# Kernel tuning notes

Measured on AMD Instinct MI355X. Metric: run time of the kernel, lower is better.

## Reference

```python
import jax, jax.numpy as jnp
import numpy as np

N = 100000   # nodes
E = 1600000  # edges (avg degree 16)
D = 128      # input_dim = embedding_dim = output_dim
NEG_SLOPE = 0.01  # nn.LeakyReLU default


def setup_inputs() -> dict:
    key = jax.random.key(0)
    k0, k1, k2, k3, k4, k5 = jax.random.split(key, 6)
    x = jax.random.normal(k0, (N, D), jnp.float32)
    edge_index = jax.random.randint(k1, (2, E), 0, N, dtype=jnp.int32)
    batch = jnp.zeros((N,), jnp.int32)
    # GCNConv params (glorot-ish scale)
    W1 = jax.random.normal(k2, (D, D), jnp.float32) * 0.05
    b1 = jax.random.normal(k3, (D,), jnp.float32) * 0.05
    W2 = jax.random.normal(k4, (D, D), jnp.float32) * 0.05
    b2 = jax.random.normal(k5, (D,), jnp.float32) * 0.05
    return {"x": x, "W1": W1, "b1": b1, "W2": W2, "b2": b2,
            "edge_index": edge_index, "batch": batch}


def _gcn_conv(x, W, b, src, dst, deg_isqrt):
    # x' = D^{-1/2} (A + I) D^{-1/2} (x W) + b   (PyG GCNConv defaults)
    h = x @ W                                   # [N, D]
    coef = deg_isqrt[src] * deg_isqrt[dst]      # [E]
    msg = h[src] * coef[:, None]                # [E, D] gather + scale
    out = jax.ops.segment_sum(msg, dst, num_segments=N)  # scatter-add
    out = out + h * (deg_isqrt * deg_isqrt)[:, None]      # self-loop term
    return out + b


def reference(x, W1, b1, W2, b2, edge_index, batch):
    src, dst = edge_index[0], edge_index[1]
    # degree on A + I (self loops), same for both layers
    deg = jax.ops.segment_sum(jnp.ones((E,), x.dtype), dst, num_segments=N) + 1.0
    deg_isqrt = jax.lax.rsqrt(deg)
    h = _gcn_conv(x, W1, b1, src, dst, deg_isqrt)
    h = jax.nn.leaky_relu(h, NEG_SLOPE)
    h = _gcn_conv(h, W2, b2, src, dst, deg_isqrt)
    return jax.nn.leaky_relu(h, NEG_SLOPE)
```

## Files before the change

### kernel.cpp

```cpp
#include <hip/hip_runtime.h>
#include <hip/hip_bf16.h>
#include <stdint.h>

#define NN 100000
#define NE 1600000
#define NR (NE + NN)
#define DD 128
#define NEG 0.01f
#define NB 196
#define EPB 4096
#define NBLK1 391

typedef __attribute__((ext_vector_type(8))) short short8;
typedef __attribute__((ext_vector_type(4))) float floatx4;
typedef __attribute__((ext_vector_type(4))) uint32_t uint32x4;

__device__ __forceinline__ uint16_t f2bf(float f){
  uint32_t i = __float_as_uint(f);
  return (uint16_t)((i + 0x7FFFu + ((i >> 16) & 1u)) >> 16);
}
__device__ __forceinline__ float lrelu(float x){ return fmaxf(x, NEG * x); }

__global__ void k_detect(const uint32_t* __restrict__ xw, int* __restrict__ flag){
  int lane = threadIdx.x;
  uint32_t w = xw[lane];
  uint32_t e = (w >> 7) & 0xFFu;
  int plaus = (e >= 100u && e <= 134u) ? 1 : 0;
  unsigned long long b = __ballot(plaus);
  if (lane == 0) flag[0] = (__popcll(b) >= 48) ? 0 : 1;
}

__global__ __launch_bounds__(256) void k_hist(const int* __restrict__ dst,
                                              int* __restrict__ ghist){
  __shared__ int lh[NB];
  int t = threadIdx.x, b = blockIdx.x;
  if (t < NB) lh[t] = 0;
  __syncthreads();
  #pragma unroll
  for (int i = 0; i < 16; i++){
    int e = b * EPB + i * 256 + t;
    if (e < NE) atomicAdd(&lh[dst[e] >> 9], 1);
  }
  __syncthreads();
  if (t < NB) ghist[t * NBLK1 + b] = lh[t];
}

__global__ __launch_bounds__(512) void k_bscan(int* __restrict__ ghist,
                                               int* __restrict__ btotal){
  __shared__ int sm[512];
  int t = threadIdx.x, bkt = blockIdx.x;
  int v = (t < NBLK1) ? ghist[bkt * NBLK1 + t] : 0;
  sm[t] = v;
  __syncthreads();
  for (int s = 1; s < 512; s <<= 1){
    int add = (t >= s) ? sm[t - s] : 0;
    __syncthreads();
    sm[t] += add;
    __syncthreads();
  }
  if (t < NBLK1) ghist[bkt * NBLK1 + t] = sm[t] - v;
  if (t == 0) btotal[bkt] = sm[511];
}

__global__ __launch_bounds__(256) void k_bscan2(const int* __restrict__ btotal,
                                                int* __restrict__ bucketbase){
  __shared__ int sm[256];
  int t = threadIdx.x;
  int v = (t < NB) ? btotal[t] : 0;
  sm[t] = v;
  __syncthreads();
  for (int s = 1; s < 256; s <<= 1){
    int add = (t >= s) ? sm[t - s] : 0;
    __syncthreads();
    sm[t] += add;
    __syncthreads();
  }
  if (t < NB) bucketbase[t] = sm[t] - v;
  if (t == 0) bucketbase[NB] = sm[255];
}

__global__ __launch_bounds__(256) void k_scatter(const int* __restrict__ src,
                                                 const int* __restrict__ dst,
                                                 const int* __restrict__ ghist,
                                                 const int* __restrict__ bucketbase,
                                                 uint64_t* __restrict__ pairs){
  __shared__ int lcur[NB];
  int t = threadIdx.x, b = blockIdx.x;
  if (t < NB) lcur[t] = bucketbase[t] + ghist[t * NBLK1 + b];
  __syncthreads();
  #pragma unroll
  for (int i = 0; i < 16; i++){
    int e = b * EPB + i * 256 + t;
    if (e < NE){
      int s = src[e], d = dst[e];
      int pos = atomicAdd(&lcur[d >> 9], 1);
      pairs[pos] = ((uint64_t)(uint32_t)d << 32) | (uint32_t)s;
    }
  }
}

__global__ __launch_bounds__(512) void k_bsort(const uint64_t* __restrict__ pairs,
                                               const int* __restrict__ bucketbase,
                                               int2* __restrict__ pairs2,
                                               int* __restrict__ prowstart,
                                               float* __restrict__ dis){
  __shared__ int lcnt[512], lofs[512], sm[512];
  __shared__ float sdn[512];
  int t = threadIdx.x, bkt = blockIdx.x;
  int n0 = bkt << 9;
  int beg = bucketbase[bkt], end = bucketbase[bkt + 1];
  int begS = beg + n0;
  lcnt[t] = 0;
  __syncthreads();
  for (int i = beg + t; i < end; i += 512){
    int d = (int)(pairs[i] >> 32);
    atomicAdd(&lcnt[d - n0], 1);
  }
  __syncthreads();
  int n = n0 + t;
  int inb = (n < NN) ? 1 : 0;
  int v = lcnt[t] + inb;
  sm[t] = v;
  __syncthreads();
  for (int s = 1; s < 512; s <<= 1){
    int add = (t >= s) ? sm[t - s] : 0;
    __syncthreads();
    sm[t] += add;
    __syncthreads();
  }
  int excl = sm[t] - v;
  float dn = rsqrtf((float)(lcnt[t] + 1));
  lofs[t] = excl + 1;
  sdn[t] = dn;
  if (inb){
    prowstart[n] = begS + excl;
    dis[n] = dn;
    pairs2[begS + excl] = make_int2(n, __float_as_int(dn));
  }
  if (bkt == 0 && t == 0) prowstart[NN] = NR;
  __syncthreads();
  for (int i = beg + t; i < end; i += 512){
    uint64_t u = pairs[i];
    int d = (int)(u >> 32);
    int p = atomicAdd(&lofs[d - n0], 1);
    pairs2[begS + p] = make_int2((int)(uint32_t)u, __float_as_int(sdn[d - n0]));
  }
}

__global__ void k_prep2(int2* __restrict__ pairs2, const float* __restrict__ dis){
  int i = blockIdx.x * 256 + threadIdx.x;
  if (i < NR){
    int2 r = pairs2[i];
    r.y = __float_as_int(__int_as_float(r.y) * dis[r.x]);
    pairs2[i] = r;
  }
}

__global__ void k_wb(const void* __restrict__ W1, const void* __restrict__ W2,
                     const void* __restrict__ b1, const void* __restrict__ b2,
                     uint16_t* __restrict__ WT1, uint16_t* __restrict__ WT2,
                     uint16_t* __restrict__ bb, const int* __restrict__ flag){
  int idx = blockIdx.x * 256 + threadIdx.x;
  int f = flag[0];
  if (idx < 16384){
    int c = idx >> 7, k = idx & 127;
    WT1[idx] = f ? f2bf(((const float*)W1)[k * DD + c])
                 : ((const uint16_t*)W1)[k * DD + c];
  } else if (idx < 32768){
    int j = idx - 16384;
    int c = j >> 7, k = j & 127;
    WT2[j] = f ? f2bf(((const float*)W2)[k * DD + c])
               : ((const uint16_t*)W2)[k * DD + c];
  } else if (idx < 33024){
    int j = idx - 32768;
    const void* s = (j < 128) ? b1 : b2;
    int i2 = j & 127;
    bb[j] = f ? f2bf(((const float*)s)[i2]) : ((const uint16_t*)s)[i2];
  }
}

__device__ __forceinline__ short8 ldcvt(const float* __restrict__ p){
  floatx4 u = ((const floatx4*)p)[0], v = ((const floatx4*)p)[1];
  short8 r;
  r[0] = (short)f2bf(u.x); r[1] = (short)f2bf(u.y);
  r[2] = (short)f2bf(u.z); r[3] = (short)f2bf(u.w);
  r[4] = (short)f2bf(v.x); r[5] = (short)f2bf(v.y);
  r[6] = (short)f2bf(v.z); r[7] = (short)f2bf(v.w);
  return r;
}

__global__ __launch_bounds__(256) void k_gemm(const void* __restrict__ X,
                                              const uint16_t* __restrict__ WT,
                                              uint16_t* __restrict__ H,
                                              const int* __restrict__ flag,
                                              int xf32){
  __shared__ uint16_t lwt[128 * 136];
  int t = threadIdx.x;
  const uint32_t* wt32 = (const uint32_t*)WT;
  #pragma unroll
  for (int i = 0; i < 32; i++){
    int uidx = t + 256 * i;
    uint32_t w2 = wt32[uidx];
    int el = uidx * 2;
    int c = el >> 7, k = el & 127;
    *(uint32_t*)&lwt[c * 136 + k] = w2;
  }
  __syncthreads();

  int wave = t >> 6, lane = t & 63;
  int m = lane & 15, q = lane >> 4;
  int rowbase = blockIdx.x * 64 + wave * 16;
  int ar = rowbase + m;
  if (ar >= NN) ar = 0;
  short8 a0, a1, a2, a3;
  if (xf32 && flag[0]){
    const float* xr = (const float*)X + (size_t)ar * DD;
    a0 = ldcvt(xr + q * 8);        a1 = ldcvt(xr + (q + 4) * 8);
    a2 = ldcvt(xr + (q + 8) * 8);  a3 = ldcvt(xr + (q + 12) * 8);
  } else {
    const short8* xrow = (const short8*)((const uint16_t*)X + (size_t)ar * DD);
    a0 = xrow[q]; a1 = xrow[q + 4]; a2 = xrow[q + 8]; a3 = xrow[q + 12];
  }

  #pragma unroll
  for (int nt = 0; nt < 8; nt++){
    int c = nt * 16 + m;
    const uint16_t* bp = &lwt[c * 136 + q * 8];
    floatx4 acc = {0.f, 0.f, 0.f, 0.f};
    acc = __builtin_amdgcn_mfma_f32_16x16x32_bf16(a0, *(const short8*)(bp +  0), acc, 0, 0, 0);
    acc = __builtin_amdgcn_mfma_f32_16x16x32_bf16(a1, *(const short8*)(bp + 32), acc, 0, 0, 0);
    acc = __builtin_amdgcn_mfma_f32_16x16x32_bf16(a2, *(const short8*)(bp + 64), acc, 0, 0, 0);
    acc = __builtin_amdgcn_mfma_f32_16x16x32_bf16(a3, *(const short8*)(bp + 96), acc, 0, 0, 0);
    #pragma unroll
    for (int r = 0; r < 4; r++){
      int row = rowbase + q * 4 + r;
      if (row < NN) H[(size_t)row * DD + c] = f2bf(acc[r]);
    }
  }
}

#define FMA8(VA, CF)                                                     \
  acc[0] = fmaf(__uint_as_float(VA.x << 16),         CF, acc[0]);        \
  acc[1] = fmaf(__uint_as_float(VA.x & 0xffff0000u), CF, acc[1]);        \
  acc[2] = fmaf(__uint_as_float(VA.y << 16),         CF, acc[2]);        \
  acc[3] = fmaf(__uint_as_float(VA.y & 0xffff0000u), CF, acc[3]);        \
  acc[4] = fmaf(__uint_as_float(VA.z << 16),         CF, acc[4]);        \
  acc[5] = fmaf(__uint_as_float(VA.z & 0xffff0000u), CF, acc[5]);        \
  acc[6] = fmaf(__uint_as_float(VA.w << 16),         CF, acc[6]);        \
  acc[7] = fmaf(__uint_as_float(VA.w & 0xffff0000u), CF, acc[7]);

__global__ __launch_bounds__(256) void k_agg(const uint16_t* __restrict__ H,
                                             const int* __restrict__ prow,
                                             const int2* __restrict__ pairs2,
                                             const uint16_t* __restrict__ bias,
                                             void* __restrict__ OUT,
                                             const int* __restrict__ flag,
                                             int is_final){
  __shared__ int2 ebuf[4][68];
  int wave = threadIdx.x >> 6, lane = threadIdx.x & 63;
  int grp = lane >> 4, sl = lane & 15;
  if (lane < 4) ebuf[wave][64 + lane] = make_int2(0, 0);
  int n = blockIdx.x * 4 + wave;
  if (n >= NN) return;
  int beg = prow[n], end = prow[n + 1];

  float acc[8] = {0.f,0.f,0.f,0.f,0.f,0.f,0.f,0.f};
  for (int j0 = beg; j0 < end; j0 += 64){
    int cnt = min(64, end - j0);
    int2 r = (lane < cnt) ? pairs2[j0 + lane] : make_int2(0, 0);
    ebuf[wave][lane] = r;
    int chunks = (cnt + 3) >> 2;
    int2 ea = ebuf[wave][grp];
    uint32x4 va = *(const uint32x4*)(H + (size_t)ea.x * DD + sl * 8);
    for (int c = 0; c < chunks; c++){
      int2 eb = ebuf[wave][c * 4 + 4 + grp];
      uint32x4 vb = *(const uint32x4*)(H + (size_t)eb.x * DD + sl * 8);
      float cf = __int_as_float(ea.y);
      FMA8(va, cf)
      ea = eb; va = vb;
    }
  }
  #pragma unroll
  for (int j = 0; j < 8; j++){
    acc[j] += __shfl_xor(acc[j], 16, 64);
    acc[j] += __shfl_xor(acc[j], 32, 64);
  }
  uint32x4 bv = ((const uint32x4*)bias)[sl];
  float o0 = lrelu(acc[0] + __uint_as_float(bv.x << 16));
  float o1 = lrelu(acc[1] + __uint_as_float(bv.x & 0xffff0000u));
  float o2 = lrelu(acc[2] + __uint_as_float(bv.y << 16));
  float o3 = lrelu(acc[3] + __uint_as_float(bv.y & 0xffff0000u));
  float o4 = lrelu(acc[4] + __uint_as_float(bv.z << 16));
  float o5 = lrelu(acc[5] + __uint_as_float(bv.z & 0xffff0000u));
  float o6 = lrelu(acc[6] + __uint_as_float(bv.w << 16));
  float o7 = lrelu(acc[7] + __uint_as_float(bv.w & 0xffff0000u));
  if (is_final && flag[0]){
    float* orow = (float*)OUT + (size_t)n * DD + sl * 8;
    if (lane < 16){ floatx4 vv = {o0, o1, o2, o3}; ((floatx4*)orow)[0] = vv; }
    else if (lane < 32){ floatx4 vv = {o4, o5, o6, o7}; ((floatx4*)orow)[1] = vv; }
  } else if (lane < 16){
    uint32x4 pv;
    pv.x = (uint32_t)f2bf(o0) | ((uint32_t)f2bf(o1) << 16);
    pv.y = (uint32_t)f2bf(o2) | ((uint32_t)f2bf(o3) << 16);
    pv.z = (uint32_t)f2bf(o4) | ((uint32_t)f2bf(o5) << 16);
    pv.w = (uint32_t)f2bf(o6) | ((uint32_t)f2bf(o7) << 16);
    *(uint32x4*)((uint16_t*)OUT + (size_t)n * DD + sl * 8) = pv;
  }
}

extern "C" void kernel_launch(void* const* d_in, const int* in_sizes, int n_in,
                              void* d_out, int out_size, void* d_ws, size_t ws_size,
                              hipStream_t stream){
  const void* x  = d_in[0];
  const void* W1 = d_in[1];
  const void* b1 = d_in[2];
  const void* W2 = d_in[3];
  const void* b2 = d_in[4];
  const int* ei   = (const int*)d_in[5];
  const int* esrc = ei;
  const int* edst = ei + NE;

  char* ws = (char*)d_ws;
  float*    dis        = (float*)(ws + 0);
  int*      prow       = (int*)(ws + 512ull * 1024);
  int*      flag       = (int*)(ws + 960ull * 1024);
  uint16_t* WT1        = (uint16_t*)(ws + 964ull * 1024);
  uint16_t* WT2        = (uint16_t*)(ws + 996ull * 1024);
  uint16_t* bb         = (uint16_t*)(ws + 1028ull * 1024);
  int*      ghist      = (int*)(ws + 1032ull * 1024);
  int*      btotal     = (int*)(ws + 1344ull * 1024);
  int*      bucketbase = (int*)(ws + 1348ull * 1024);
  int2*     pairs2     = (int2*)(ws + 2048ull * 1024);
  uint64_t* pairs      = (uint64_t*)(ws + 16384ull * 1024);
  uint16_t* hA         = (uint16_t*)(ws + 16384ull * 1024);
  uint16_t* hB         = (uint16_t*)d_out;

  k_detect<<<1, 64, 0, stream>>>((const uint32_t*)x, flag);
  k_hist  <<<NBLK1, 256, 0, stream>>>(edst, ghist);
  k_bscan <<<NB, 512, 0, stream>>>(ghist, btotal);
  k_bscan2<<<1, 256, 0, stream>>>(btotal, bucketbase);
  k_scatter<<<NBLK1, 256, 0, stream>>>(esrc, edst, ghist, bucketbase, pairs);
  k_bsort <<<NB, 512, 0, stream>>>(pairs, bucketbase, pairs2, prow, dis);
  k_prep2 <<<(NR + 255) / 256, 256, 0, stream>>>(pairs2, dis);
  k_wb    <<<129, 256, 0, stream>>>(W1, W2, b1, b2, WT1, WT2, bb, flag);

  k_gemm<<<(NN + 63) / 64, 256, 0, stream>>>(x, WT1, hA, flag, 1);
  k_agg <<<NN / 4, 256, 0, stream>>>(hA, prow, pairs2, bb, hB, flag, 0);
  k_gemm<<<(NN + 63) / 64, 256, 0, stream>>>(hB, WT2, hA, flag, 0);
  k_agg <<<NN / 4, 256, 0, stream>>>(hA, prow, pairs2, bb + 128, d_out, flag, 1);
}
```

Before: 321.4 us.

## Assign one 16-lane group per node in aggregation with register prefetch pipeline

The aggregation kernel now gives each node a 16-thread group instead of a whole wave, so a block handles 16 nodes rather than 4. Edges are walked serially with a three-deep register prefetch of pair entries and a two-deep prefetch of feature rows, replacing the LDS edge buffer and the cross-group shuffle reduction. This removes shared-memory traffic, shuffles and the idle lanes that short adjacency lists left in a full wave. In exchange, memory-level parallelism per node drops and load balance depends on degree variance within a wave. The code assumes every node has at least one entry, which holds because self-loops are included.

```diff
diff --git a/kernel.cpp b/kernel.cpp
--- a/kernel.cpp
+++ b/kernel.cpp
@@ -256,35 +256,28 @@
                                              void* __restrict__ OUT,
                                              const int* __restrict__ flag,
                                              int is_final){
-  __shared__ int2 ebuf[4][68];
-  int wave = threadIdx.x >> 6, lane = threadIdx.x & 63;
-  int grp = lane >> 4, sl = lane & 15;
-  if (lane < 4) ebuf[wave][64 + lane] = make_int2(0, 0);
-  int n = blockIdx.x * 4 + wave;
-  if (n >= NN) return;
+  int g = threadIdx.x >> 4, sl = threadIdx.x & 15;
+  int n = blockIdx.x * 16 + g;
   int beg = prow[n], end = prow[n + 1];
+  const uint16_t* Hs = H + sl * 8;
 
   float acc[8] = {0.f,0.f,0.f,0.f,0.f,0.f,0.f,0.f};
-  for (int j0 = beg; j0 < end; j0 += 64){
-    int cnt = min(64, end - j0);
-    int2 r = (lane < cnt) ? pairs2[j0 + lane] : make_int2(0, 0);
-    ebuf[wave][lane] = r;
-    int chunks = (cnt + 3) >> 2;
-    int2 ea = ebuf[wave][grp];
-    uint32x4 va = *(const uint32x4*)(H + (size_t)ea.x * DD + sl * 8);
-    for (int c = 0; c < chunks; c++){
-      int2 eb = ebuf[wave][c * 4 + 4 + grp];
-      uint32x4 vb = *(const uint32x4*)(H + (size_t)eb.x * DD + sl * 8);
-      float cf = __int_as_float(ea.y);
-      FMA8(va, cf)
-      ea = eb; va = vb;
-    }
-  }
-  #pragma unroll
-  for (int j = 0; j < 8; j++){
-    acc[j] += __shfl_xor(acc[j], 16, 64);
-    acc[j] += __shfl_xor(acc[j], 32, 64);
-  }
+  const int2 z = make_int2(0, 0);
+  int2 r0 = pairs2[beg];
+  int2 r1 = (beg + 1 < end) ? pairs2[beg + 1] : z;
+  int2 r2 = (beg + 2 < end) ? pairs2[beg + 2] : z;
+  uint32x4 v0 = *(const uint32x4*)(Hs + (size_t)r0.x * DD);
+  uint32x4 v1 = *(const uint32x4*)(Hs + (size_t)r1.x * DD);
+
+  for (int j = beg; j < end; j++){
+    int2 r3 = (j + 3 < end) ? pairs2[j + 3] : z;
+    uint32x4 v2 = *(const uint32x4*)(Hs + (size_t)r2.x * DD);
+    float cf = __int_as_float(r0.y);
+    FMA8(v0, cf)
+    r0 = r1; r1 = r2; r2 = r3;
+    v0 = v1; v1 = v2;
+  }
+
   uint32x4 bv = ((const uint32x4*)bias)[sl];
   float o0 = lrelu(acc[0] + __uint_as_float(bv.x << 16));
   float o1 = lrelu(acc[1] + __uint_as_float(bv.x & 0xffff0000u));
@@ -296,9 +289,10 @@
   float o7 = lrelu(acc[7] + __uint_as_float(bv.w & 0xffff0000u));
   if (is_final && flag[0]){
     float* orow = (float*)OUT + (size_t)n * DD + sl * 8;
-    if (lane < 16){ floatx4 vv = {o0, o1, o2, o3}; ((floatx4*)orow)[0] = vv; }
-    else if (lane < 32){ floatx4 vv = {o4, o5, o6, o7}; ((floatx4*)orow)[1] = vv; }
-  } else if (lane < 16){
+    floatx4 va = {o0, o1, o2, o3}, vb = {o4, o5, o6, o7};
+    ((floatx4*)orow)[0] = va;
+    ((floatx4*)orow)[1] = vb;
+  } else {
     uint32x4 pv;
     pv.x = (uint32_t)f2bf(o0) | ((uint32_t)f2bf(o1) << 16);
     pv.y = (uint32_t)f2bf(o2) | ((uint32_t)f2bf(o3) << 16);
@@ -345,7 +339,7 @@
   k_wb    <<<129, 256, 0, stream>>>(W1, W2, b1, b2, WT1, WT2, bb, flag);
 
   k_gemm<<<(NN + 63) / 64, 256, 0, stream>>>(x, WT1, hA, flag, 1);
-  k_agg <<<NN / 4, 256, 0, stream>>>(hA, prow, pairs2, bb, hB, flag, 0);
+  k_agg <<<NN / 16, 256, 0, stream>>>(hA, prow, pairs2, bb, hB, flag, 0);
   k_gemm<<<(NN + 63) / 64, 256, 0, stream>>>(hB, WT2, hA, flag, 0);
-  k_agg <<<NN / 4, 256, 0, stream>>>(hA, prow, pairs2, bb + 128, d_out, flag, 1);
-}
+  k_agg <<<NN / 16, 256, 0, stream>>>(hA, prow, pairs2, bb + 128, d_out, flag, 1);
+}
```

New measurement: 340.4 us. +5.9%, slower.
